# Performance work log

Hardware: AMD Instinct MI355X
Metric: run time of the kernel (lower is better)

The kernel has to match this reference:

```python
import jax, jax.numpy as jnp
import numpy as np

N, E, F_IN, H, C, G = 100000, 3200000, 256, 256, 10, 128
EPS = 1e-5


def _seg_sum(data, ids, n):
    return jax.ops.segment_sum(data, ids, num_segments=n)


def gcn_conv(x, W, b, src, dst, n):
    # PyG GCNConv: h = x @ W; add self-loops; sym-normalize by deg^{-1/2}; scatter-add; + bias
    h = x @ W  # [N, H]
    loop = jnp.arange(n)
    s = jnp.concatenate([src, loop])
    d = jnp.concatenate([dst, loop])
    deg = _seg_sum(jnp.ones(s.shape[0], dtype=h.dtype), d, n)  # in-degree incl. self-loop
    dis = jnp.where(deg > 0, jax.lax.rsqrt(deg), 0.0)
    norm = dis[s] * dis[d]  # [E+N]
    out = _seg_sum(h[s] * norm[:, None], d, n)  # gather -> scale -> scatter-add
    return out + b


def batch_norm(x, gamma, beta):
    # training-mode BN over the node/graph axis (biased variance, as torch)
    mean = jnp.mean(x, axis=0)
    var = jnp.var(x, axis=0)
    return (x - mean) * jax.lax.rsqrt(var + EPS) * gamma + beta


def setup_inputs() -> dict:
    key = jax.random.key(0)
    ks = jax.random.split(key, 16)
    inp = {
        "x": jax.random.normal(ks[0], (N, F_IN), dtype=jnp.float32),
        "edge_index": jax.random.randint(ks[1], (2, E), 0, N, dtype=jnp.int64)
        if jax.config.jax_enable_x64 else jax.random.randint(ks[1], (2, E), 0, N, dtype=jnp.int32),
        "batch": jnp.sort(jax.random.randint(ks[2], (N,), 0, G)),
    }
    dims_in = [F_IN, H, H]
    for i in range(3):
        scale = 1.0 / np.sqrt(dims_in[i])
        inp[f"W{i}"] = jax.random.normal(ks[3 + i], (dims_in[i], H), dtype=jnp.float32) * scale
        inp[f"b{i}"] = jnp.zeros((H,), dtype=jnp.float32)
        inp[f"g{i}"] = jnp.ones((H,), dtype=jnp.float32)
        inp[f"be{i}"] = jnp.zeros((H,), dtype=jnp.float32)
    inp["lin1_w"] = jax.random.normal(ks[8], (H, H), dtype=jnp.float32) / np.sqrt(H)
    inp["lin1_b"] = jnp.zeros((H,), dtype=jnp.float32)
    inp["bn1_g"] = jnp.ones((H,), dtype=jnp.float32)
    inp["bn1_b"] = jnp.zeros((H,), dtype=jnp.float32)
    inp["lin2_w"] = jax.random.normal(ks[9], (H, C), dtype=jnp.float32) / np.sqrt(H)
    inp["lin2_b"] = jnp.zeros((C,), dtype=jnp.float32)
    return inp


def reference(x, edge_index, batch,
              W0, b0, g0, be0, W1, b1, g1, be1, W2, b2, g2, be2,
              lin1_w, lin1_b, bn1_g, bn1_b, lin2_w, lin2_b):
    src, dst = edge_index[0], edge_index[1]
    Ws = [(W0, b0, g0, be0), (W1, b1, g1, be1), (W2, b2, g2, be2)]
    h = x
    for (W, b, g, be) in Ws:
        h = jax.nn.relu(batch_norm(gcn_conv(h, W, b, src, dst, N), g, be))
    # global mean pool over graphs
    sums = _seg_sum(h, batch, G)                                  # [G, H]
    cnt = _seg_sum(jnp.ones((N,), dtype=h.dtype), batch, G)       # [G]
    pooled = sums / jnp.maximum(cnt, 1.0)[:, None]
    z = jax.nn.relu(batch_norm(pooled @ lin1_w + lin1_b, bn1_g, bn1_b))
    # dropout is identity in eval mode
    return z @ lin2_w + lin2_b  # [G, C]
```

## Files before the change

kernel.cpp:

```cpp
#include <hip/hip_runtime.h>

#define N_NODES 100000
#define N_EDGES 3200000
#define HD      256
#define NGRAPH  128
#define NCLASS  10
#define BN_EPS  1e-5f

typedef unsigned short u16;
typedef __attribute__((ext_vector_type(4))) float f32x4;
typedef __attribute__((ext_vector_type(8))) float f32x8;
typedef __attribute__((ext_vector_type(8))) short bf16x8;
typedef __attribute__((ext_vector_type(8))) u16   u16x8;
typedef __attribute__((ext_vector_type(4))) u16   u16x4;

__device__ __forceinline__ float b2f(u16 u){ return __uint_as_float(((unsigned)u) << 16); }
__device__ __forceinline__ u16 f2b(float f){
  unsigned x = __float_as_uint(f);
  x += 0x7fffu + ((x >> 16) & 1u);
  return (u16)(x >> 16);
}
__device__ __forceinline__ f32x4 c4(u16x4 v){
  f32x4 r = { b2f(v[0]), b2f(v[1]), b2f(v[2]), b2f(v[3]) };
  return r;
}
__device__ __forceinline__ f32x8 c8(u16x8 v){
  f32x8 r = { b2f(v[0]), b2f(v[1]), b2f(v[2]), b2f(v[3]),
              b2f(v[4]), b2f(v[5]), b2f(v[6]), b2f(v[7]) };
  return r;
}


__global__ __launch_bounds__(256) void cvt_k(const float* __restrict__ x, u16* __restrict__ xb){
  size_t i = ((size_t)blockIdx.x * 256 + threadIdx.x) * 8;
  f32x4 v0 = *(const f32x4*)(x + i);
  f32x4 v1 = *(const f32x4*)(x + i + 4);
  u16x8 o = { f2b(v0[0]), f2b(v0[1]), f2b(v0[2]), f2b(v0[3]),
              f2b(v1[0]), f2b(v1[1]), f2b(v1[2]), f2b(v1[3]) };
  *(u16x8*)(xb + i) = o;
}

__global__ __launch_bounds__(256) void wt_k(const float* __restrict__ W, u16* __restrict__ Wt){
  int i = blockIdx.x * 256 + threadIdx.x;
  int k = i >> 8, n = i & 255;
  Wt[n * HD + k] = f2b(W[k * HD + n]);
}

__global__ __launch_bounds__(256) void cnt_k(const int* __restrict__ ei, int* __restrict__ cnt){
  int e = blockIdx.x * 256 + threadIdx.x;
  if (e < N_EDGES) atomicAdd(&cnt[ei[N_EDGES + e]], 1);
}

__global__ __launch_bounds__(256) void scan1_k(const int* __restrict__ cnt, int* __restrict__ tmp,
                                               int* __restrict__ bsum){
  __shared__ int sh[256];
  int tid = threadIdx.x;
  int i = blockIdx.x * 256 + tid;
  int v = (i < N_NODES) ? cnt[i] : 0;
  sh[tid] = v;
  __syncthreads();
  #pragma unroll
  for (int off = 1; off < 256; off <<= 1){
    int t = (tid >= off) ? sh[tid - off] : 0;
    __syncthreads();
    sh[tid] += t;
    __syncthreads();
  }
  if (i < N_NODES) tmp[i] = sh[tid];
  if (tid == 255) bsum[blockIdx.x] = sh[255];
}

__global__ __launch_bounds__(512) void scan2_k(const int* __restrict__ bsum, int* __restrict__ boff, int nb){
  __shared__ int sh[512];
  int tid = threadIdx.x;
  int v = (tid < nb) ? bsum[tid] : 0;
  sh[tid] = v;
  __syncthreads();
  for (int off = 1; off < 512; off <<= 1){
    int t = (tid >= off) ? sh[tid - off] : 0;
    __syncthreads();
    sh[tid] += t;
    __syncthreads();
  }
  if (tid < nb) boff[tid] = sh[tid] - v;
}

__global__ __launch_bounds__(256) void scan3_k(const int* __restrict__ tmp, const int* __restrict__ boff,
                                               int* __restrict__ rowptr){
  int i = blockIdx.x * 256 + threadIdx.x;
  if (i > N_NODES) return;
  if (i == 0) rowptr[0] = 0;
  else rowptr[i] = tmp[i - 1] + boff[(i - 1) >> 8];
}

__global__ __launch_bounds__(256) void fill_k(const int* __restrict__ ei, const int* __restrict__ rowptr,
                                              int* __restrict__ fill, int* __restrict__ colx){
  int e = blockIdx.x * 256 + threadIdx.x;
  if (e < N_EDGES){
    int d = ei[N_EDGES + e];
    int pos = atomicAdd(&fill[d], 1);
    colx[rowptr[d] + pos] = ei[e];
  }
}

__global__ __launch_bounds__(256) void dis_k(const int* __restrict__ cnt, float* __restrict__ dis){
  int i = blockIdx.x * 256 + threadIdx.x;
  if (i < N_NODES) dis[i] = rsqrtf((float)(cnt[i] + 1));
}


__device__ __forceinline__ int swzoff(int row, int kel){
  return (row * 512 + kel * 2) ^ ((row & 7) << 4);
}

__global__ __launch_bounds__(256) void gemm_k(const u16* __restrict__ X, const u16* __restrict__ Wt,
                                              const float* __restrict__ dis, u16* __restrict__ HN)
{
  __shared__ u16x8 AsV[2048];
  __shared__ u16x8 BsV[2048];
  char* As = (char*)AsV;
  char* Bs = (char*)BsV;
  int tid = threadIdx.x;
  int colbase = blockIdx.x * 64;
  int rowbase = blockIdx.y * 64;
  {
    int r = tid >> 2, q = tid & 3;
    int grow = rowbase + r;
    const u16* src = X + (size_t)grow * HD + q * 64;
    #pragma unroll
    for (int j = 0; j < 8; ++j){
      u16x8 v = {0,0,0,0,0,0,0,0};
      if (grow < N_NODES) v = *(const u16x8*)(src + j * 8);
      *(u16x8*)(As + swzoff(r, q * 64 + j * 8)) = v;
    }
    const u16* wsrc = Wt + (size_t)(colbase + r) * HD + q * 64;
    #pragma unroll
    for (int j = 0; j < 8; ++j)
      *(u16x8*)(Bs + swzoff(r, q * 64 + j * 8)) = *(const u16x8*)(wsrc + j * 8);
  }
  __syncthreads();

  int w = tid >> 6, lane = tid & 63;
  int wm = w >> 1, wn = w & 1;
  int lr = lane & 15, lg = lane >> 4;

  f32x4 acc00 = {0,0,0,0}, acc01 = {0,0,0,0}, acc10 = {0,0,0,0}, acc11 = {0,0,0,0};
  #pragma unroll
  for (int ks = 0; ks < 8; ++ks){
    int ka = ks * 32 + lg * 8;
    bf16x8 a0 = *(const bf16x8*)(As + swzoff(wm * 32 + lr,      ka));
    bf16x8 a1 = *(const bf16x8*)(As + swzoff(wm * 32 + 16 + lr, ka));
    bf16x8 b0 = *(const bf16x8*)(Bs + swzoff(wn * 32 + lr,      ka));
    bf16x8 b1 = *(const bf16x8*)(Bs + swzoff(wn * 32 + 16 + lr, ka));
    acc00 = __builtin_amdgcn_mfma_f32_16x16x32_bf16(a0, b0, acc00, 0, 0, 0);
    acc01 = __builtin_amdgcn_mfma_f32_16x16x32_bf16(a0, b1, acc01, 0, 0, 0);
    acc10 = __builtin_amdgcn_mfma_f32_16x16x32_bf16(a1, b0, acc10, 0, 0, 0);
    acc11 = __builtin_amdgcn_mfma_f32_16x16x32_bf16(a1, b1, acc11, 0, 0, 0);
  }

  #pragma unroll
  for (int mt = 0; mt < 2; ++mt){
    f32x4 ac0 = mt ? acc10 : acc00;
    f32x4 ac1 = mt ? acc11 : acc01;
    #pragma unroll
    for (int r = 0; r < 4; ++r){
      int grow = rowbase + wm * 32 + mt * 16 + lg * 4 + r;
      if (grow < N_NODES){
        float dd = dis[grow];
        size_t base = (size_t)grow * HD + colbase + wn * 32 + lr;
        HN[base]      = f2b(ac0[r] * dd);
        HN[base + 16] = f2b(ac1[r] * dd);
      }
    }
  }
}


__global__ __launch_bounds__(256) void agg_k(const u16* __restrict__ HN, const int* __restrict__ rowptr,
                                             const int* __restrict__ colx, const float* __restrict__ dis,
                                             u16* __restrict__ OUTB)
{
  int wid = threadIdx.x >> 6, lane = threadIdx.x & 63;
  int node = blockIdx.x * 8 + wid * 2 + (lane >> 5);
  int c0 = (lane & 31) * 8;
  const u16* base = HN + (size_t)c0;

  f32x8 a0 = {0,0,0,0,0,0,0,0}, a1 = a0, a2 = a0, a3 = a0;
  int e = rowptr[node], end = rowptr[node + 1];
  for (; e + 4 <= end; e += 4){
    int s0 = colx[e], s1 = colx[e + 1], s2 = colx[e + 2], s3 = colx[e + 3];
    u16x8 v0 = *(const u16x8*)(base + (size_t)s0 * HD);
    u16x8 v1 = *(const u16x8*)(base + (size_t)s1 * HD);
    u16x8 v2 = *(const u16x8*)(base + (size_t)s2 * HD);
    u16x8 v3 = *(const u16x8*)(base + (size_t)s3 * HD);
    a0 += c8(v0); a1 += c8(v1); a2 += c8(v2); a3 += c8(v3);
  }
  for (; e < end; ++e)
    a0 += c8(*(const u16x8*)(base + (size_t)colx[e] * HD));
  a0 += c8(*(const u16x8*)(base + (size_t)node * HD));
  f32x8 res = ((a0 + a1) + (a2 + a3)) * dis[node];
  u16x8 o = { f2b(res[0]), f2b(res[1]), f2b(res[2]), f2b(res[3]),
              f2b(res[4]), f2b(res[5]), f2b(res[6]), f2b(res[7]) };
  *(u16x8*)(OUTB + (size_t)node * HD + c0) = o;
}


__global__ __launch_bounds__(256) void stat_k(const u16* __restrict__ OUTB, float* __restrict__ sums){
  int c = threadIdx.x;
  float s = 0.f, q = 0.f;
  for (int r = blockIdx.x; r < N_NODES; r += gridDim.x){
    float v = b2f(OUTB[(size_t)r * HD + c]);
    s += v; q += v * v;
  }
  atomicAdd(&sums[c], s);
  atomicAdd(&sums[HD + c], q);
}

__global__ __launch_bounds__(256) void prep_k(const float* __restrict__ sums, const float* __restrict__ gamma,
                                              const float* __restrict__ beta, float* __restrict__ prm){
  int c = threadIdx.x;
  float mean = sums[c] / (float)N_NODES;
  float var  = fmaxf(sums[HD + c] / (float)N_NODES - mean * mean, 0.f);
  float inv  = rsqrtf(var + BN_EPS);
  float a = gamma[c] * inv;
  prm[c] = a;
  prm[HD + c] = beta[c] - mean * a;
}

__global__ __launch_bounds__(256) void norm_k(const u16* __restrict__ OUTB, const float* __restrict__ prm,
                                              u16* __restrict__ XB){
  size_t i = (size_t)blockIdx.x * 256 + threadIdx.x;
  int cq = (int)(i & 63);
  size_t base = i * 4;
  f32x4 v = c4(*(const u16x4*)(OUTB + base));
  f32x4 a = *(const f32x4*)(prm + cq * 4);
  f32x4 b = *(const f32x4*)(prm + HD + cq * 4);
  f32x4 y = v * a + b;
  u16x4 o = { f2b(fmaxf(y[0], 0.f)), f2b(fmaxf(y[1], 0.f)),
              f2b(fmaxf(y[2], 0.f)), f2b(fmaxf(y[3], 0.f)) };
  *(u16x4*)(XB + base) = o;
}


__global__ __launch_bounds__(256) void bnd2_k(const int* __restrict__ batch, int* __restrict__ gs,
                                              int* __restrict__ ge){
  int i = blockIdx.x * 256 + threadIdx.x;
  if (i >= N_NODES) return;
  int b = batch[i];
  if (i == 0) gs[b] = 0;
  else {
    int p = batch[i - 1];
    if (p != b){ ge[p] = i; gs[b] = i; }
  }
  if (i == N_NODES - 1) ge[b] = N_NODES;
}

__global__ __launch_bounds__(256) void pool_k(const u16* __restrict__ xb, const int* __restrict__ gs,
                                              const int* __restrict__ ge, float* __restrict__ pooled){
  __shared__ float red[4][HD];
  int g = blockIdx.x;
  int s = gs[g], e = ge[g];
  int w = threadIdx.x >> 6;
  int c0 = (threadIdx.x & 63) * 4;
  f32x4 acc = {0,0,0,0};
  for (int r = s + w; r < e; r += 4){
    u16x4 v = *(const u16x4*)(xb + (size_t)r * HD + c0);
    acc += c4(v);
  }
  *(f32x4*)&red[w][c0] = acc;
  __syncthreads();
  if (w == 0){
    f32x4 t = *(f32x4*)&red[0][c0];
    t += *(f32x4*)&red[1][c0];
    t += *(f32x4*)&red[2][c0];
    t += *(f32x4*)&red[3][c0];
    float cntf = (e > s) ? (float)(e - s) : 1.0f;
    *(f32x4*)(pooled + g * HD + c0) = t * (1.0f / cntf);
  }
}

__global__ __launch_bounds__(256) void lin1_k(const float* __restrict__ pooled, const float* __restrict__ w,
                                              const float* __restrict__ b, float* __restrict__ z1){
  __shared__ float pr[HD];
  int g = blockIdx.x, c = threadIdx.x;
  pr[c] = pooled[g * HD + c];
  __syncthreads();
  float acc = b[c];
  #pragma unroll 8
  for (int k = 0; k < HD; ++k) acc = fmaf(pr[k], w[k * HD + c], acc);
  z1[g * HD + c] = acc;
}

__global__ __launch_bounds__(256) void bn1_k(float* __restrict__ z1, const float* __restrict__ g,
                                             const float* __restrict__ b){
  int c = threadIdx.x;
  float s = 0.f, q = 0.f;
  for (int r = 0; r < NGRAPH; ++r){
    float v = z1[r * HD + c];
    s += v; q += v * v;
  }
  float mean = s / (float)NGRAPH;
  float var  = fmaxf(q / (float)NGRAPH - mean * mean, 0.f);
  float inv  = rsqrtf(var + BN_EPS);
  float a = g[c] * inv, sh = b[c] - mean * a;
  for (int r = 0; r < NGRAPH; ++r)
    z1[r * HD + c] = fmaxf(z1[r * HD + c] * a + sh, 0.f);
}

__global__ __launch_bounds__(256) void lin2_k(const float* __restrict__ z1, const float* __restrict__ w,
                                              const float* __restrict__ b, float* __restrict__ out){
  __shared__ float zr[HD];
  int g = blockIdx.x;
  zr[threadIdx.x] = z1[g * HD + threadIdx.x];
  __syncthreads();
  if (threadIdx.x < NCLASS){
    float acc = b[threadIdx.x];
    #pragma unroll 8
    for (int k = 0; k < HD; ++k) acc = fmaf(zr[k], w[k * NCLASS + threadIdx.x], acc);
    out[g * NCLASS + threadIdx.x] = acc;
  }
}


extern "C" void kernel_launch(void* const* d_in, const int* in_sizes, int n_in,
                              void* d_out, int out_size, void* d_ws, size_t ws_size,
                              hipStream_t stream)
{
  const float* x      = (const float*)d_in[0];
  const int*   ei     = (const int*)d_in[1];
  const int*   batch  = (const int*)d_in[2];
  const float* W[3]   = {(const float*)d_in[3], (const float*)d_in[7], (const float*)d_in[11]};
  const float* gam[3] = {(const float*)d_in[5], (const float*)d_in[9], (const float*)d_in[13]};
  const float* bet[3] = {(const float*)d_in[6], (const float*)d_in[10], (const float*)d_in[14]};
  const float* lin1_w = (const float*)d_in[15];
  const float* lin1_b = (const float*)d_in[16];
  const float* bn1_g  = (const float*)d_in[17];
  const float* bn1_b  = (const float*)d_in[18];
  const float* lin2_w = (const float*)d_in[19];
  const float* lin2_b = (const float*)d_in[20];
  float* out = (float*)d_out;

  char* ws = (char*)d_ws;
  size_t off = 0;
  auto alloc = [&](size_t bytes) -> void* {
    void* p = ws + off;
    off = (off + bytes + 255) & ~(size_t)255;
    return p;
  };
  u16*   xb     = (u16*)alloc((size_t)N_NODES * HD * 2);
  u16*   hn     = (u16*)alloc((size_t)N_NODES * HD * 2);
  u16*   outb   = (u16*)alloc((size_t)N_NODES * HD * 2);
  u16*   wt     = (u16*)alloc((size_t)3 * HD * HD * 2);
  int*   cnt    = (int*)alloc((size_t)N_NODES * 4);
  int*   fill   = (int*)alloc((size_t)N_NODES * 4);
  int*   rowptr = (int*)alloc((size_t)(N_NODES + 1) * 4);
  int*   tmp    = (int*)alloc((size_t)N_NODES * 4);
  int*   bsum   = (int*)alloc(512 * 4);
  int*   boff   = (int*)alloc(512 * 4);
  int*   colx   = (int*)alloc((size_t)N_EDGES * 4);
  float* dis    = (float*)alloc((size_t)N_NODES * 4);
  float* bnsum  = (float*)alloc(2 * HD * 4);
  float* prm    = (float*)alloc(2 * HD * 4);
  int*   gs     = (int*)alloc(NGRAPH * 4);
  int*   ge     = (int*)alloc(NGRAPH * 4);
  float* pooled = (float*)alloc((size_t)NGRAPH * HD * 4);
  float* z1     = (float*)alloc((size_t)NGRAPH * HD * 4);
  (void)ws_size; (void)n_in; (void)in_sizes; (void)out_size;

  const int NB1 = (N_NODES + 255) / 256;

  hipMemsetAsync(cnt, 0, (size_t)N_NODES * 4, stream);
  hipMemsetAsync(fill, 0, (size_t)N_NODES * 4, stream);

  cvt_k<<<12500, 256, 0, stream>>>(x, xb);
  for (int l = 0; l < 3; ++l)
    wt_k<<<256, 256, 0, stream>>>(W[l], wt + (size_t)l * HD * HD);

  cnt_k<<<12500, 256, 0, stream>>>(ei, cnt);
  scan1_k<<<NB1, 256, 0, stream>>>(cnt, tmp, bsum);
  scan2_k<<<1, 512, 0, stream>>>(bsum, boff, NB1);
  scan3_k<<<(N_NODES + 256) / 256 + 1, 256, 0, stream>>>(tmp, boff, rowptr);
  fill_k<<<12500, 256, 0, stream>>>(ei, rowptr, fill, colx);
  dis_k<<<NB1, 256, 0, stream>>>(cnt, dis);

  for (int l = 0; l < 3; ++l){
    gemm_k<<<dim3(4, 1563), 256, 0, stream>>>(xb, wt + (size_t)l * HD * HD, dis, hn);
    agg_k<<<12500, 256, 0, stream>>>(hn, rowptr, colx, dis, outb);
    hipMemsetAsync(bnsum, 0, 2 * HD * 4, stream);
    stat_k<<<1024, 256, 0, stream>>>(outb, bnsum);
    prep_k<<<1, 256, 0, stream>>>(bnsum, gam[l], bet[l], prm);
    norm_k<<<25000, 256, 0, stream>>>(outb, prm, xb);
  }

  hipMemsetAsync(gs, 0x7f, NGRAPH * 4, stream);
  hipMemsetAsync(ge, 0, NGRAPH * 4, stream);
  bnd2_k<<<NB1, 256, 0, stream>>>(batch, gs, ge);
  pool_k<<<NGRAPH, 256, 0, stream>>>(xb, gs, ge, pooled);
  lin1_k<<<NGRAPH, 256, 0, stream>>>(pooled, lin1_w, lin1_b, z1);
  bn1_k<<<1, 256, 0, stream>>>(z1, bn1_g, bn1_b);
  lin2_k<<<NGRAPH, 256, 0, stream>>>(z1, lin2_w, lin2_b, out);
}
```

Baseline: 1.568 ms.

## Fuse BN+ReLU into GEMM load and pooling; split aggregation by column halves

Removes the standalone normalize kernel. The BatchNorm affine and ReLU are now applied while the next layer's GEMM loads its A tile, and inside the final pooling kernel, which saves a full read and write of the activations per layer. Aggregation runs as two launches, each covering half of the feature columns with 16 lanes per node, to shrink the gather working set for better cache locality. The stat kernel grid is also reduced. The cost is extra per-element arithmetic in the GEMM prologue and a second pass over the edge lists.

Measured after the change: 1.816 ms. +15.8%, slower.

```diff
diff --git a/kernel.cpp b/kernel.cpp
--- a/kernel.cpp
+++ b/kernel.cpp
@@ -114,7 +114,8 @@
 }
 
 __global__ __launch_bounds__(256) void gemm_k(const u16* __restrict__ X, const u16* __restrict__ Wt,
-                                              const float* __restrict__ dis, u16* __restrict__ HN)
+                                              const float* __restrict__ dis, const float* __restrict__ prm,
+                                              int useprm, u16* __restrict__ HN)
 {
   __shared__ u16x8 AsV[2048];
   __shared__ u16x8 BsV[2048];
@@ -131,6 +132,13 @@
     for (int j = 0; j < 8; ++j){
       u16x8 v = {0,0,0,0,0,0,0,0};
       if (grow < N_NODES) v = *(const u16x8*)(src + j * 8);
+      if (useprm){
+        f32x8 a = *(const f32x8*)(prm + q * 64 + j * 8);
+        f32x8 b = *(const f32x8*)(prm + HD + q * 64 + j * 8);
+        f32x8 y = c8(v) * a + b;
+        #pragma unroll
+        for (int t = 0; t < 8; ++t) v[t] = f2b(fmaxf(y[t], 0.f));
+      }
       *(u16x8*)(As + swzoff(r, q * 64 + j * 8)) = v;
     }
     const u16* wsrc = Wt + (size_t)(colbase + r) * HD + q * 64;
@@ -176,13 +184,13 @@
 }
 
 
-__global__ __launch_bounds__(256) void agg_k(const u16* __restrict__ HN, const int* __restrict__ rowptr,
-                                             const int* __restrict__ colx, const float* __restrict__ dis,
-                                             u16* __restrict__ OUTB)
+__global__ __launch_bounds__(256) void agg2_k(const u16* __restrict__ HN, const int* __restrict__ rowptr,
+                                              const int* __restrict__ colx, const float* __restrict__ dis,
+                                              u16* __restrict__ OUTB, int colbase)
 {
   int wid = threadIdx.x >> 6, lane = threadIdx.x & 63;
-  int node = blockIdx.x * 8 + wid * 2 + (lane >> 5);
-  int c0 = (lane & 31) * 8;
+  int node = blockIdx.x * 16 + wid * 4 + (lane >> 4);
+  int c0 = colbase + (lane & 15) * 8;
   const u16* base = HN + (size_t)c0;
 
   f32x8 a0 = {0,0,0,0,0,0,0,0}, a1 = a0, a2 = a0, a3 = a0;
@@ -227,20 +235,6 @@
   prm[HD + c] = beta[c] - mean * a;
 }
 
-__global__ __launch_bounds__(256) void norm_k(const u16* __restrict__ OUTB, const float* __restrict__ prm,
-                                              u16* __restrict__ XB){
-  size_t i = (size_t)blockIdx.x * 256 + threadIdx.x;
-  int cq = (int)(i & 63);
-  size_t base = i * 4;
-  f32x4 v = c4(*(const u16x4*)(OUTB + base));
-  f32x4 a = *(const f32x4*)(prm + cq * 4);
-  f32x4 b = *(const f32x4*)(prm + HD + cq * 4);
-  f32x4 y = v * a + b;
-  u16x4 o = { f2b(fmaxf(y[0], 0.f)), f2b(fmaxf(y[1], 0.f)),
-              f2b(fmaxf(y[2], 0.f)), f2b(fmaxf(y[3], 0.f)) };
-  *(u16x4*)(XB + base) = o;
-}
-
 
 __global__ __launch_bounds__(256) void bnd2_k(const int* __restrict__ batch, int* __restrict__ gs,
                                               int* __restrict__ ge){
@@ -255,17 +249,23 @@
   if (i == N_NODES - 1) ge[b] = N_NODES;
 }
 
-__global__ __launch_bounds__(256) void pool_k(const u16* __restrict__ xb, const int* __restrict__ gs,
-                                              const int* __restrict__ ge, float* __restrict__ pooled){
+__global__ __launch_bounds__(256) void pool_k(const u16* __restrict__ outb, const float* __restrict__ prm,
+                                              const int* __restrict__ gs, const int* __restrict__ ge,
+                                              float* __restrict__ pooled){
   __shared__ float red[4][HD];
   int g = blockIdx.x;
   int s = gs[g], e = ge[g];
   int w = threadIdx.x >> 6;
   int c0 = (threadIdx.x & 63) * 4;
+  f32x4 pa = *(const f32x4*)(prm + c0);
+  f32x4 pb = *(const f32x4*)(prm + HD + c0);
   f32x4 acc = {0,0,0,0};
   for (int r = s + w; r < e; r += 4){
-    u16x4 v = *(const u16x4*)(xb + (size_t)r * HD + c0);
-    acc += c4(v);
+    f32x4 v = c4(*(const u16x4*)(outb + (size_t)r * HD + c0));
+    f32x4 y = v * pa + pb;
+    y[0] = fmaxf(y[0], 0.f); y[1] = fmaxf(y[1], 0.f);
+    y[2] = fmaxf(y[2], 0.f); y[3] = fmaxf(y[3], 0.f);
+    acc += y;
   }
   *(f32x4*)&red[w][c0] = acc;
   __syncthreads();
@@ -384,18 +384,19 @@
   dis_k<<<NB1, 256, 0, stream>>>(cnt, dis);
 
   for (int l = 0; l < 3; ++l){
-    gemm_k<<<dim3(4, 1563), 256, 0, stream>>>(xb, wt + (size_t)l * HD * HD, dis, hn);
-    agg_k<<<12500, 256, 0, stream>>>(hn, rowptr, colx, dis, outb);
+    const u16* gin = (l == 0) ? xb : outb;
+    gemm_k<<<dim3(4, 1563), 256, 0, stream>>>(gin, wt + (size_t)l * HD * HD, dis, prm, l > 0, hn);
+    agg2_k<<<6250, 256, 0, stream>>>(hn, rowptr, colx, dis, outb, 0);
+    agg2_k<<<6250, 256, 0, stream>>>(hn, rowptr, colx, dis, outb, 128);
     hipMemsetAsync(bnsum, 0, 2 * HD * 4, stream);
-    stat_k<<<1024, 256, 0, stream>>>(outb, bnsum);
+    stat_k<<<256, 256, 0, stream>>>(outb, bnsum);
     prep_k<<<1, 256, 0, stream>>>(bnsum, gam[l], bet[l], prm);
-    norm_k<<<25000, 256, 0, stream>>>(outb, prm, xb);
   }
 
   hipMemsetAsync(gs, 0x7f, NGRAPH * 4, stream);
   hipMemsetAsync(ge, 0, NGRAPH * 4, stream);
   bnd2_k<<<NB1, 256, 0, stream>>>(batch, gs, ge);
-  pool_k<<<NGRAPH, 256, 0, stream>>>(xb, gs, ge, pooled);
+  pool_k<<<NGRAPH, 256, 0, stream>>>(outb, prm, gs, ge, pooled);
   lin1_k<<<NGRAPH, 256, 0, stream>>>(pooled, lin1_w, lin1_b, z1);
   bn1_k<<<1, 256, 0, stream>>>(z1, bn1_g, bn1_b);
   lin2_k<<<NGRAPH, 256, 0, stream>>>(z1, lin2_w, lin2_b, out);
```
